# Optimization experiments

Hardware: AMD Instinct MI355X
Metric: run time of the kernel (lower is better)

Reference implementation:

```python
import jax, jax.numpy as jnp
import numpy as np

B, T, SZ, H = 16, 512, 512, 8
HD = SZ // H
D0, STD, GAMMA = 6.3, 1.4, 2.0
MAX_RPE = 16

def _dwconv(x, w):
    # depthwise conv1d, kernel 5, pad 2, groups=C, no bias; x: [B,T,C], w: [C,1,5]
    y = jax.lax.conv_general_dilated(x.transpose(0, 2, 1), w, (1,), [(2, 2)],
        dimension_numbers=('NCH', 'OIH', 'NCH'), feature_group_count=x.shape[-1])
    return y.transpose(0, 2, 1)

def _forward(mask, key, value, query, Wq, bq, Wk, bk, Wv, bv, Wcq, Wck, Wcv, Wgq, bgq, Wgk, bgk, Wgv, bgv, WmD, bmD, rpe_table, Wo, bo):
    q = query @ Wq.T + bq
    k = key @ Wk.T + bk
    v = value @ Wv.T + bv
    xn = key  # x_norm := key in the original forward
    # gated depthwise-conv context injection (qkv_context=[1,1,1], fuse='gate')
    qc = _dwconv(xn, Wcq)
    g = jax.nn.sigmoid(jnp.concatenate([q, qc], -1) @ Wgq.T + bgq)
    q = (1 - g) * q + g * qc
    kc = _dwconv(xn, Wck)
    g = jax.nn.sigmoid(jnp.concatenate([k, kc], -1) @ Wgk.T + bgk)
    k = (1 - g) * k + g * kc
    vc = _dwconv(xn, Wcv)
    g = jax.nn.sigmoid(jnp.concatenate([v, vc], -1) @ Wgv.T + bgv)
    v = (1 - g) * v + g * vc
    # learned Gaussian width: mod_D='head_share', mod_src='Q'
    off = (q @ WmD.T + bmD)[..., 0]                       # [B,T]
    m_D = D0 + 2.0 * STD * jnp.tanh(off / GAMMA)          # [B,T]
    qh = q.reshape(B, T, H, HD).transpose(0, 2, 1, 3) / jnp.sqrt(jnp.float32(HD))
    kh = k.reshape(B, T, H, HD).transpose(0, 2, 1, 3)
    vh = v.reshape(B, T, H, HD).transpose(0, 2, 1, 3)
    scores = jnp.einsum('bhqd,bhkd->bhqk', qh, kh)        # [B,H,T,T]
    idx = jnp.arange(T)
    d_int = idx[:, None] - idx[None, :]                   # i - j
    rd = jnp.clip(-d_int, -MAX_RPE, MAX_RPE) + MAX_RPE    # rpe indices [T,T]
    rpe = rpe_table[rd]                                   # [T,T,2*HD]
    rpe_k, rpe_v = rpe[..., :HD], rpe[..., HD:]
    scores = scores + jnp.einsum('bhqd,qkd->bhqk', qh, rpe_k)
    dist = d_int.astype(jnp.float32)
    scores = scores - dist ** 2 / (m_D[:, None, :, None] ** 2 / 2.0)
    scores = jnp.where(mask[:, None, :, :], -jnp.inf, scores)
    attn = jax.nn.softmax(scores, axis=-1)                # dropout is identity at eval
    ctx = jnp.einsum('bhqk,bhkd->bhqd', attn, vh) + jnp.einsum('bhqk,qkd->bhqd', attn, rpe_v)
    out = ctx.transpose(0, 2, 1, 3).reshape(B, T, SZ) @ Wo.T + bo
    return out

def setup_inputs():
    rng = jax.random.key(0)
    ks = jax.random.split(rng, 20)
    s = 0.02
    lin = lambda k, o, i: jax.random.normal(k, (o, i), jnp.float32) * s
    lengths = jax.random.randint(ks[3], (B,), T // 2, T + 1)
    mask = (jnp.arange(T)[None, :] >= lengths[:, None])[:, None, :]  # [B,1,T], True = pad
    return {
        'key': jax.random.normal(ks[0], (B, T, SZ), jnp.float32),
        'value': jax.random.normal(ks[1], (B, T, SZ), jnp.float32),
        'query': jax.random.normal(ks[2], (B, T, SZ), jnp.float32),
        'mask': mask,
        'Wq': lin(ks[4], SZ, SZ), 'bq': jnp.zeros((SZ,), jnp.float32),
        'Wk': lin(ks[5], SZ, SZ), 'bk': jnp.zeros((SZ,), jnp.float32),
        'Wv': lin(ks[6], SZ, SZ), 'bv': jnp.zeros((SZ,), jnp.float32),
        'Wcq': jax.random.normal(ks[7], (SZ, 1, 5), jnp.float32) * s,
        'Wck': jax.random.normal(ks[8], (SZ, 1, 5), jnp.float32) * s,
        'Wcv': jax.random.normal(ks[9], (SZ, 1, 5), jnp.float32) * s,
        'Wgq': lin(ks[10], 1, 2 * SZ), 'bgq': jnp.zeros((1,), jnp.float32),
        'Wgk': lin(ks[11], 1, 2 * SZ), 'bgk': jnp.zeros((1,), jnp.float32),
        'Wgv': lin(ks[12], 1, 2 * SZ), 'bgv': jnp.zeros((1,), jnp.float32),
        'WmD': lin(ks[13], 1, SZ), 'bmD': jnp.zeros((1,), jnp.float32),
        'rpe_table': jax.random.normal(ks[14], (2 * MAX_RPE + 1, 2 * HD), jnp.float32) * s,
        'Wo': lin(ks[15], SZ, SZ), 'bo': jnp.zeros((SZ,), jnp.float32),
    }

def reference(key, value, query, mask, Wq, bq, Wk, bk, Wv, bv, Wcq, Wck, Wcv, Wgq, bgq, Wgk, bgk, Wgv, bgv, WmD, bmD, rpe_table, Wo, bo):
    return _forward(mask, key, value, query, Wq, bq, Wk, bk, Wv, bv, Wcq, Wck, Wcv, Wgq, bgq, Wgk, bgk, Wgv, bgv, WmD, bmD, rpe_table, Wo, bo)
```

## Files before the change

kernel.cpp:

```cpp
#include <hip/hip_runtime.h>
#include <math.h>

#define NB 16
#define NT 512
#define NSZ 512
#define NH 8
#define NHD 64
#define MAXR 16

#define C_D0 6.3f
#define C_STD 1.4f
#define C_GAMMA 2.0f

#define NEGINF (-1e30f)
#define LOG2E 1.4426950408889634f
#define C1F   0.18033688011112042f

typedef unsigned short u16;
typedef __attribute__((ext_vector_type(8))) short bf16x8;
typedef __attribute__((ext_vector_type(4))) float f32x4;
typedef __attribute__((ext_vector_type(8))) unsigned short u16x8;

__device__ __forceinline__ u16 f2b(float f) {
    union { float f; unsigned int u; } c; c.f = f;
    unsigned int u = c.u + 0x7FFFu + ((c.u >> 16) & 1u);
    return (u16)(u >> 16);
}
__device__ __forceinline__ float b2f(u16 h) {
    union { unsigned int u; float f; } c; c.u = ((unsigned int)h) << 16;
    return c.f;
}

#if __has_builtin(__builtin_amdgcn_exp2f)
__device__ __forceinline__ float exp2_fast(float x) { return __builtin_amdgcn_exp2f(x); }
#else
__device__ __forceinline__ float exp2_fast(float x) { return exp2f(x); }
#endif

#define GL2LDS(gp, lp) __builtin_amdgcn_global_load_lds( \
    (const __attribute__((address_space(1))) void*)(gp), \
    (__attribute__((address_space(3))) void*)(lp), 16, 0, 0)

#define SWU(r, c) ((((r) * 8) + ((c) ^ ((r) & 7))) * 8)

__global__ __launch_bounds__(256) void cvt4_bf16(
    const float* __restrict__ s0, const float* __restrict__ s1,
    const float* __restrict__ s2, const float* __restrict__ s3,
    u16* __restrict__ d0, u16* __restrict__ d1,
    u16* __restrict__ d2, u16* __restrict__ d3, int n)
{
    const float* s; u16* d;
    switch (blockIdx.y) {
        case 0: s = s0; d = d0; break;
        case 1: s = s1; d = d1; break;
        case 2: s = s2; d = d2; break;
        default: s = s3; d = d3; break;
    }
    int i = (blockIdx.x * 256 + threadIdx.x) * 8;
    if (i >= n) return;
    float4 a = *(const float4*)&s[i];
    float4 b = *(const float4*)&s[i + 4];
    u16x8 v;
    v[0]=f2b(a.x); v[1]=f2b(a.y); v[2]=f2b(a.z); v[3]=f2b(a.w);
    v[4]=f2b(b.x); v[5]=f2b(b.y); v[6]=f2b(b.z); v[7]=f2b(b.w);
    *(u16x8*)&d[i] = v;
}

__global__ __launch_bounds__(256) void wprep(
    const float* __restrict__ Wcq, const float* __restrict__ Wck,
    const float* __restrict__ Wcv, float* __restrict__ WcT)
{
    const int z = blockIdx.y;
    const float* src = z == 0 ? Wcq : (z == 1 ? Wck : Wcv);
    int idx = blockIdx.x * 256 + threadIdx.x;
    if (idx >= 2560) return;
    int c = idx / 5, j = idx % 5;
    WcT[(size_t)z * 2560 + j * 512 + c] = src[idx];
}

__global__ __launch_bounds__(256) void gemm_qkv(
    const float* __restrict__ A0, const float* __restrict__ A1, const float* __restrict__ A2,
    const u16* __restrict__ Wc,
    const float* __restrict__ bq, const float* __restrict__ bk, const float* __restrict__ bv,
    u16* __restrict__ pkv)
{
    __shared__ u16 Al[128 * 32];
    __shared__ u16 Bl[128 * 32];
    const int z = blockIdx.z;
    const float* A = z == 0 ? A0 : (z == 1 ? A1 : A2);
    const u16* W = Wc + (size_t)z * NSZ * NSZ;
    const float* bias = z == 0 ? bq : (z == 1 ? bk : bv);
    const int tid = threadIdx.x;
    const int m0 = blockIdx.x * 128;
    const int n0 = blockIdx.y * 128;
    const int w = tid >> 6, lane = tid & 63;
    const int wm = (w >> 1) * 64, wn = (w & 1) * 64;
    const int fr = lane & 15, fk = lane >> 4;

    f32x4 acc[4][4] = {};
    for (int k0 = 0; k0 < NSZ; k0 += 32) {
        float4 a0[2], a1[2];
        #pragma unroll
        for (int p = 0; p < 2; ++p) {
            int s = tid + p * 256;
            int row = s >> 2, cb = s & 3;
            const float* ga = &A[(size_t)(m0 + row) * NSZ + k0 + cb * 8];
            a0[p] = *(const float4*)ga;
            a1[p] = *(const float4*)(ga + 4);
            GL2LDS(&W[(size_t)(n0 + row) * NSZ + k0 + cb * 8], &Bl[s * 8]);
        }
        #pragma unroll
        for (int p = 0; p < 2; ++p) {
            int s = tid + p * 256;
            u16x8 v;
            v[0]=f2b(a0[p].x); v[1]=f2b(a0[p].y); v[2]=f2b(a0[p].z); v[3]=f2b(a0[p].w);
            v[4]=f2b(a1[p].x); v[5]=f2b(a1[p].y); v[6]=f2b(a1[p].z); v[7]=f2b(a1[p].w);
            *(u16x8*)&Al[s * 8] = v;
        }
        __syncthreads();
        bf16x8 af[4], bfr[4];
        #pragma unroll
        for (int mf = 0; mf < 4; ++mf)
            af[mf] = *(const bf16x8*)&Al[(wm + mf * 16 + fr) * 32 + fk * 8];
        #pragma unroll
        for (int nf = 0; nf < 4; ++nf)
            bfr[nf] = *(const bf16x8*)&Bl[(wn + nf * 16 + fr) * 32 + fk * 8];
        #pragma unroll
        for (int mf = 0; mf < 4; ++mf)
            #pragma unroll
            for (int nf = 0; nf < 4; ++nf)
                acc[mf][nf] = __builtin_amdgcn_mfma_f32_16x16x32_bf16(
                    af[mf], bfr[nf], acc[mf][nf], 0, 0, 0);
        __syncthreads();
    }
    #pragma unroll
    for (int mf = 0; mf < 4; ++mf) {
        #pragma unroll
        for (int nf = 0; nf < 4; ++nf) {
            int col = n0 + wn + nf * 16 + fr;
            float bvv = bias[col];
            #pragma unroll
            for (int r = 0; r < 4; ++r) {
                int rowg = m0 + wm + mf * 16 + fk * 4 + r;
                pkv[(size_t)rowg * 1536 + z * 512 + col] = f2b(acc[mf][nf][r] + bvv);
            }
        }
    }
}

__global__ __launch_bounds__(256) void gemm_out(
    const u16* __restrict__ A, const u16* __restrict__ W,
    const float* __restrict__ bias, float* __restrict__ Cout, int M, int N, int K)
{
    __shared__ u16 Al[64 * 32];
    __shared__ u16 Bl[128 * 32];
    const int tid = threadIdx.x;
    const int m0 = blockIdx.x * 64;
    const int n0 = blockIdx.y * 128;
    const int w = tid >> 6, lane = tid & 63;
    const int wm = (w >> 1) * 32, wn = (w & 1) * 64;
    const int fr = lane & 15, fk = lane >> 4;

    f32x4 acc[2][4] = {};
    for (int k0 = 0; k0 < K; k0 += 32) {
        {
            int row = tid >> 2, cb = tid & 3;
            GL2LDS(&A[(size_t)(m0 + row) * K + k0 + cb * 8], &Al[tid * 8]);
        }
        #pragma unroll
        for (int p = 0; p < 2; ++p) {
            int s = tid + p * 256;
            int row = s >> 2, cb = s & 3;
            GL2LDS(&W[(size_t)(n0 + row) * K + k0 + cb * 8], &Bl[s * 8]);
        }
        __syncthreads();
        bf16x8 af[2], bfr[4];
        #pragma unroll
        for (int mf = 0; mf < 2; ++mf)
            af[mf] = *(const bf16x8*)&Al[(wm + mf * 16 + fr) * 32 + fk * 8];
        #pragma unroll
        for (int nf = 0; nf < 4; ++nf)
            bfr[nf] = *(const bf16x8*)&Bl[(wn + nf * 16 + fr) * 32 + fk * 8];
        #pragma unroll
        for (int mf = 0; mf < 2; ++mf)
            #pragma unroll
            for (int nf = 0; nf < 4; ++nf)
                acc[mf][nf] = __builtin_amdgcn_mfma_f32_16x16x32_bf16(
                    af[mf], bfr[nf], acc[mf][nf], 0, 0, 0);
        __syncthreads();
    }
    #pragma unroll
    for (int mf = 0; mf < 2; ++mf) {
        #pragma unroll
        for (int nf = 0; nf < 4; ++nf) {
            int col = n0 + wn + nf * 16 + fr;
            float bv = bias[col];
            #pragma unroll
            for (int r = 0; r < 4; ++r) {
                int rowg = m0 + wm + mf * 16 + fk * 4 + r;
                Cout[(size_t)rowg * N + col] = acc[mf][nf][r] + bv;
            }
        }
    }
}

__global__ void conv_gate_all(
    const float* __restrict__ xn, u16* __restrict__ pkv,
    const float* __restrict__ WcT,
    const float* __restrict__ Wgq, const float* __restrict__ bgq,
    const float* __restrict__ Wgk, const float* __restrict__ bgk,
    const float* __restrict__ Wgv, const float* __restrict__ bgv,
    const float* __restrict__ WmD, const float* __restrict__ bmD,
    float* __restrict__ mD)
{
    const int w = threadIdx.x >> 6, lane = threadIdx.x & 63;
    const int bt = blockIdx.x * 4 + w;
    const int b = bt >> 9, tpos = bt & (NT - 1);
    const int c0 = lane * 8;

    float x[5][8];
    #pragma unroll
    for (int j = 0; j < 5; ++j) {
        int tt = tpos + j - 2;
        if (tt >= 0 && tt < NT) {
            const float4* xp = (const float4*)&xn[((size_t)(b*NT + tt))*NSZ + c0];
            float4 u0 = xp[0], u1 = xp[1];
            x[j][0]=u0.x; x[j][1]=u0.y; x[j][2]=u0.z; x[j][3]=u0.w;
            x[j][4]=u1.x; x[j][5]=u1.y; x[j][6]=u1.z; x[j][7]=u1.w;
        } else {
            #pragma unroll
            for (int i = 0; i < 8; ++i) x[j][i] = 0.f;
        }
    }
    float aq[8] = {}, ak[8] = {}, av[8] = {};
    #pragma unroll
    for (int j = 0; j < 5; ++j) {
        const float* wq = &WcT[j * 512 + c0];
        const float* wk = &WcT[2560 + j * 512 + c0];
        const float* wv = &WcT[5120 + j * 512 + c0];
        float4 q0 = *(const float4*)wq, q1 = *(const float4*)(wq + 4);
        float4 k0 = *(const float4*)wk, k1 = *(const float4*)(wk + 4);
        float4 v0 = *(const float4*)wv, v1 = *(const float4*)(wv + 4);
        float wq8[8] = {q0.x,q0.y,q0.z,q0.w,q1.x,q1.y,q1.z,q1.w};
        float wk8[8] = {k0.x,k0.y,k0.z,k0.w,k1.x,k1.y,k1.z,k1.w};
        float wv8[8] = {v0.x,v0.y,v0.z,v0.w,v1.x,v1.y,v1.z,v1.w};
        #pragma unroll
        for (int i = 0; i < 8; ++i) {
            aq[i] += x[j][i] * wq8[i];
            ak[i] += x[j][i] * wk8[i];
            av[i] += x[j][i] * wv8[i];
        }
    }
    const size_t rb = (size_t)bt * 1536;
    u16x8 q8 = *(const u16x8*)&pkv[rb + c0];
    u16x8 k8 = *(const u16x8*)&pkv[rb + 512 + c0];
    u16x8 v8 = *(const u16x8*)&pkv[rb + 1024 + c0];

    float gql[8], gqh[8], gkl[8], gkh[8], gvl[8], gvh[8];
    {
        float4 a0 = *(const float4*)&Wgq[c0],      a1 = *(const float4*)&Wgq[c0 + 4];
        float4 a2 = *(const float4*)&Wgq[512 + c0], a3 = *(const float4*)&Wgq[512 + c0 + 4];
        gql[0]=a0.x;gql[1]=a0.y;gql[2]=a0.z;gql[3]=a0.w;gql[4]=a1.x;gql[5]=a1.y;gql[6]=a1.z;gql[7]=a1.w;
        gqh[0]=a2.x;gqh[1]=a2.y;gqh[2]=a2.z;gqh[3]=a2.w;gqh[4]=a3.x;gqh[5]=a3.y;gqh[6]=a3.z;gqh[7]=a3.w;
        float4 b0 = *(const float4*)&Wgk[c0],      b1 = *(const float4*)&Wgk[c0 + 4];
        float4 b2 = *(const float4*)&Wgk[512 + c0], b3 = *(const float4*)&Wgk[512 + c0 + 4];
        gkl[0]=b0.x;gkl[1]=b0.y;gkl[2]=b0.z;gkl[3]=b0.w;gkl[4]=b1.x;gkl[5]=b1.y;gkl[6]=b1.z;gkl[7]=b1.w;
        gkh[0]=b2.x;gkh[1]=b2.y;gkh[2]=b2.z;gkh[3]=b2.w;gkh[4]=b3.x;gkh[5]=b3.y;gkh[6]=b3.z;gkh[7]=b3.w;
        float4 c0v = *(const float4*)&Wgv[c0],      c1v = *(const float4*)&Wgv[c0 + 4];
        float4 c2v = *(const float4*)&Wgv[512 + c0], c3v = *(const float4*)&Wgv[512 + c0 + 4];
        gvl[0]=c0v.x;gvl[1]=c0v.y;gvl[2]=c0v.z;gvl[3]=c0v.w;gvl[4]=c1v.x;gvl[5]=c1v.y;gvl[6]=c1v.z;gvl[7]=c1v.w;
        gvh[0]=c2v.x;gvh[1]=c2v.y;gvh[2]=c2v.z;gvh[3]=c2v.w;gvh[4]=c3v.x;gvh[5]=c3v.y;gvh[6]=c3v.z;gvh[7]=c3v.w;
    }
    float sq = 0.f, sk = 0.f, sv = 0.f;
    #pragma unroll
    for (int i = 0; i < 8; ++i) {
        sq += b2f(q8[i]) * gql[i] + aq[i] * gqh[i];
        sk += b2f(k8[i]) * gkl[i] + ak[i] * gkh[i];
        sv += b2f(v8[i]) * gvl[i] + av[i] * gvh[i];
    }
    #pragma unroll
    for (int o = 1; o < 64; o <<= 1) {
        sq += __shfl_xor(sq, o, 64);
        sk += __shfl_xor(sk, o, 64);
        sv += __shfl_xor(sv, o, 64);
    }
    float gq = 1.f / (1.f + expf(-(sq + bgq[0])));
    float gk = 1.f / (1.f + expf(-(sk + bgk[0])));
    float gv = 1.f / (1.f + expf(-(sv + bgv[0])));

    float wm8[8];
    {
        float4 m0 = *(const float4*)&WmD[c0], m1 = *(const float4*)&WmD[c0 + 4];
        wm8[0]=m0.x;wm8[1]=m0.y;wm8[2]=m0.z;wm8[3]=m0.w;wm8[4]=m1.x;wm8[5]=m1.y;wm8[6]=m1.z;wm8[7]=m1.w;
    }
    u16x8 oq8, ok8, ov8;
    float smd = 0.f;
    #pragma unroll
    for (int i = 0; i < 8; ++i) {
        float oq = (1.f - gq) * b2f(q8[i]) + gq * aq[i];
        oq8[i] = f2b(oq);
        ok8[i] = f2b((1.f - gk) * b2f(k8[i]) + gk * ak[i]);
        ov8[i] = f2b((1.f - gv) * b2f(v8[i]) + gv * av[i]);
        smd += oq * wm8[i];
    }
    *(u16x8*)&pkv[rb + c0]        = oq8;
    *(u16x8*)&pkv[rb + 512 + c0]  = ok8;
    *(u16x8*)&pkv[rb + 1024 + c0] = ov8;
    #pragma unroll
    for (int o = 1; o < 64; o <<= 1) smd += __shfl_xor(smd, o, 64);
    if (lane == 0)
        mD[bt] = C_D0 + 2.f * C_STD * tanhf((smd + bmD[0]) / C_GAMMA);
}

__global__ __launch_bounds__(256) void vtrans(
    const u16* __restrict__ pkv, u16* __restrict__ vpT)
{
    __shared__ u16 lt[64][72];
    const int t0 = blockIdx.x * 64;
    const int h = blockIdx.y, b = blockIdx.z;
    const int tid = threadIdx.x;
    #pragma unroll
    for (int p = 0; p < 2; ++p) {
        int s = tid + p * 256;
        int t = s >> 3, c8 = s & 7;
        u16x8 v = *(const u16x8*)&pkv[((size_t)(b*NT + t0 + t))*1536 + 1024 + h*NHD + c8*8];
        *(u16x8*)&lt[t][c8 * 8] = v;
    }
    __syncthreads();
    #pragma unroll
    for (int p = 0; p < 2; ++p) {
        int s = tid + p * 256;
        int d = s >> 3, c8 = s & 7;
        u16x8 o;
        #pragma unroll
        for (int j = 0; j < 8; ++j) o[j] = lt[c8 * 8 + j][d];
        *(u16x8*)&vpT[((size_t)((b*NH + h)*NHD + d))*NT + t0 + c8*8] = o;
    }
}

__global__ __launch_bounds__(256) void attn_mfma(
    const u16* __restrict__ pkv, const u16* __restrict__ vpT,
    const float* __restrict__ mD, const int* __restrict__ mask,
    const float* __restrict__ rpe, u16* __restrict__ cxh)
{
    __shared__ __align__(16) char smem[38144];
    u16*  QP    = (u16*)(smem);
    u16*  Kl    = (u16*)(smem + 8192);
    u16*  Vl    = (u16*)(smem + 16384);
    u16*  rpk   = (u16*)(smem + 16384);
    u16*  rvl16 = (u16*)(smem + 8192);
    u16*  qdrl  = (u16*)(smem + 24576);
    float* wbufl= (float*)(smem + 29184);
    float* inv2s= (float*)(smem + 37888);

    const int tid  = threadIdx.x;
    const int lane = tid & 63;
    const int w    = tid >> 6;
    const int wq0  = w * 16;
    const int fr   = lane & 15;
    const int fq   = lane >> 4;
    const int b    = blockIdx.x >> 3;
    const int h    = blockIdx.x & 7;
    const int q0   = blockIdx.y * 64;

    const size_t qbase  = ((size_t)(b*NT + q0)) * 1536 + h * NHD;
    const size_t kbaseg = ((size_t)b * NT) * 1536 + 512 + h * NHD;
    const size_t vbaseg = ((size_t)((b*NH + h) * NHD)) * NT;

    int Lm = 512;
    #pragma unroll
    for (int j = 0; j < 8; ++j) {
        if (mask[b * NT + lane + 64 * j]) Lm = min(Lm, lane + 64 * j);
    }
    #pragma unroll
    for (int o = 1; o < 64; o <<= 1) Lm = min(Lm, __shfl_xor(Lm, o, 64));
    const int L = Lm;
    const int w0 = max(0, min(q0 - 32, L - 128));

    int r_[2], cs_[2];
    u16x8 qreg[2], kreg[2], vreg[2];
    #pragma unroll
    for (int p = 0; p < 2; ++p) {
        int s = tid + p * 256;
        r_[p] = s >> 3; cs_[p] = s & 7;
        qreg[p] = *(const u16x8*)(pkv + qbase  + (size_t)r_[p] * 1536 + cs_[p] * 8);
        kreg[p] = *(const u16x8*)(pkv + kbaseg + (size_t)(w0 + r_[p]) * 1536 + cs_[p] * 8);
        vreg[p] = *(const u16x8*)(vpT + vbaseg + (size_t)r_[p] * NT + w0 + cs_[p] * 8);
    }
    #pragma unroll
    for (int p = 0; p < 2; ++p) {
        *(u16x8*)(QP + SWU(r_[p], cs_[p])) = qreg[p];
        *(u16x8*)(Kl + SWU(r_[p], cs_[p])) = kreg[p];
    }
    for (int idx = tid; idx < 264; idx += 256) {
        int r = idx >> 3, c = idx & 7;
        float4 f0 = *(const float4*)&rpe[r * 128 + c * 8];
        float4 f1 = *(const float4*)&rpe[r * 128 + c * 8 + 4];
        u16x8 vv;
        vv[0]=f2b(f0.x); vv[1]=f2b(f0.y); vv[2]=f2b(f0.z); vv[3]=f2b(f0.w);
        vv[4]=f2b(f1.x); vv[5]=f2b(f1.y); vv[6]=f2b(f1.z); vv[7]=f2b(f1.w);
        *(u16x8*)(rpk + SWU(r, c)) = vv;
    }
    if (tid < 120) {
        u16x8 vv = {0,0,0,0,0,0,0,0};
        *(u16x8*)(rpk + (((33 + (tid >> 3)) * 8) + (tid & 7)) * 8) = vv;
    }
    if (tid < 64) {
        float md = mD[b * NT + q0 + tid];
        inv2s[tid] = 2.f * LOG2E / (md * md);
    }
    for (int i = tid; i < 64 * 34; i += 256) wbufl[i] = 0.f;
    __syncthreads();

    bf16x8 aq0 = *(const bf16x8*)(QP + SWU(wq0 + fr, fq));
    bf16x8 aq1 = *(const bf16x8*)(QP + SWU(wq0 + fr, 4 + fq));

    {
        f32x4 qd[3] = {};
        #pragma unroll
        for (int nf = 0; nf < 3; ++nf) {
            bf16x8 b0 = *(const bf16x8*)(rpk + SWU(nf * 16 + fr, fq));
            bf16x8 b1 = *(const bf16x8*)(rpk + SWU(nf * 16 + fr, 4 + fq));
            qd[nf] = __builtin_amdgcn_mfma_f32_16x16x32_bf16(aq0, b0, qd[nf], 0, 0, 0);
            qd[nf] = __builtin_amdgcn_mfma_f32_16x16x32_bf16(aq1, b1, qd[nf], 0, 0, 0);
        }
        #pragma unroll
        for (int nf = 0; nf < 3; ++nf) {
            int rd = nf * 16 + fr;
            if (rd < 33) {
                #pragma unroll
                for (int r = 0; r < 4; ++r)
                    qdrl[(wq0 + fq * 4 + r) * 36 + rd] = f2b(qd[nf][r]);
            }
        }
    }
    __syncthreads();
    #pragma unroll
    for (int p = 0; p < 2; ++p)
        *(u16x8*)(Vl + SWU(r_[p], cs_[p])) = vreg[p];

    f32x4 O[4] = {};
    float m2[4] = {NEGINF, NEGINF, NEGINF, NEGINF};
    float li[4] = {};

    #pragma unroll
    for (int t = 0; t < 2; ++t) {
        const int kb = w0 + t * 64;
        const bool pre = (t == 0);
        u16x8 kreg2[2], vreg2[2];
        if (pre) {
            const int kn = kb + 64;
            #pragma unroll
            for (int p = 0; p < 2; ++p) {
                kreg2[p] = *(const u16x8*)(pkv + kbaseg + (size_t)(kn + r_[p]) * 1536 + cs_[p] * 8);
                vreg2[p] = *(const u16x8*)(vpT + vbaseg + (size_t)r_[p] * NT + kn + cs_[p] * 8);
            }
        }
        int mk[4];
        #pragma unroll
        for (int nf = 0; nf < 4; ++nf) mk[nf] = (kb + nf * 16 + fr) >= L;

        f32x4 s_[4] = {};
        #pragma unroll
        for (int nf = 0; nf < 4; ++nf) {
            bf16x8 b0 = *(const bf16x8*)(Kl + SWU(nf * 16 + fr, fq));
            bf16x8 b1 = *(const bf16x8*)(Kl + SWU(nf * 16 + fr, 4 + fq));
            s_[nf] = __builtin_amdgcn_mfma_f32_16x16x32_bf16(aq0, b0, s_[nf], 0, 0, 0);
            s_[nf] = __builtin_amdgcn_mfma_f32_16x16x32_bf16(aq1, b1, s_[nf], 0, 0, 0);
        }
        const bool leftfar  = (kb + 79 <= q0);
        const bool rightfar = (kb >= q0 + 79);
        const bool mid = !leftfar && !rightfar;

        float p_[4][4], alpha[4], rsum_[4], ls_[4], rs_[4];
        #pragma unroll
        for (int r = 0; r < 4; ++r) {
            const int lq = wq0 + fq * 4 + r;
            const int qg = q0 + lq;
            const float iv = inv2s[lq];
            const float qf = leftfar ? b2f(qdrl[lq * 36]) : (rightfar ? b2f(qdrl[lq * 36 + 32]) : 0.f);
            float mx = NEGINF;
            #pragma unroll
            for (int nf = 0; nf < 4; ++nf) {
                const int kg = kb + nf * 16 + fr;
                float sc;
                if (mk[nf]) sc = NEGINF;
                else {
                    float qr = mid ? b2f(qdrl[lq * 36 + (min(max(kg - qg, -MAXR), MAXR) + MAXR)]) : qf;
                    float fd = (float)(qg - kg);
                    sc = (s_[nf][r] + qr) * C1F - fd * fd * iv;
                }
                p_[r][nf] = sc;
                mx = fmaxf(mx, sc);
            }
            mx = fmaxf(mx, __shfl_xor(mx, 1, 64));
            mx = fmaxf(mx, __shfl_xor(mx, 2, 64));
            mx = fmaxf(mx, __shfl_xor(mx, 4, 64));
            mx = fmaxf(mx, __shfl_xor(mx, 8, 64));
            float mn = fmaxf(m2[r], mx);
            alpha[r] = exp2_fast(m2[r] - mn);
            m2[r] = mn;
            float rsum = 0.f, ls = 0.f, rs = 0.f;
            #pragma unroll
            for (int nf = 0; nf < 4; ++nf) {
                float pv = exp2_fast(p_[r][nf] - mn);
                p_[r][nf] = pv;
                rsum += pv;
                if (mid) {
                    int kg = kb + nf * 16 + fr;
                    if (kg <= qg - MAXR) ls += pv;
                    else if (kg >= qg + MAXR) rs += pv;
                }
            }
            rsum += __shfl_xor(rsum, 1, 64); rsum += __shfl_xor(rsum, 2, 64);
            rsum += __shfl_xor(rsum, 4, 64); rsum += __shfl_xor(rsum, 8, 64);
            if (mid) {
                ls += __shfl_xor(ls, 1, 64); ls += __shfl_xor(ls, 2, 64);
                ls += __shfl_xor(ls, 4, 64); ls += __shfl_xor(ls, 8, 64);
                rs += __shfl_xor(rs, 1, 64); rs += __shfl_xor(rs, 2, 64);
                rs += __shfl_xor(rs, 4, 64); rs += __shfl_xor(rs, 8, 64);
            }
            li[r] = li[r] * alpha[r] + rsum;
            rsum_[r] = rsum; ls_[r] = ls; rs_[r] = rs;
        }
        #pragma unroll
        for (int nf = 0; nf < 4; ++nf) {
            O[nf][0] *= alpha[0]; O[nf][1] *= alpha[1];
            O[nf][2] *= alpha[2]; O[nf][3] *= alpha[3];
        }
        #pragma unroll
        for (int r = 0; r < 4; ++r) {
            int lq = wq0 + fq * 4 + r;
            if (alpha[r] != 1.f) {
                for (int c = fr; c < 33; c += 16) wbufl[lq * 34 + c] *= alpha[r];
            }
        }
        if (fr == 0) {
            #pragma unroll
            for (int r = 0; r < 4; ++r) {
                int lq = wq0 + fq * 4 + r;
                if (leftfar)       wbufl[lq * 34]      += rsum_[r];
                else if (rightfar) wbufl[lq * 34 + 32] += rsum_[r];
                else { wbufl[lq * 34] += ls_[r]; wbufl[lq * 34 + 32] += rs_[r]; }
            }
        }
        if (mid) {
            #pragma unroll
            for (int r = 0; r < 4; ++r) {
                int lq = wq0 + fq * 4 + r, qg = q0 + lq;
                #pragma unroll
                for (int nf = 0; nf < 4; ++nf) {
                    int d = kb + nf * 16 + fr - qg;
                    if (d > -MAXR && d < MAXR) wbufl[lq * 34 + d + MAXR] += p_[r][nf];
                }
            }
        }
        #pragma unroll
        for (int r = 0; r < 4; ++r) {
            int lq = wq0 + fq * 4 + r;
            #pragma unroll
            for (int nf = 0; nf < 4; ++nf) {
                int k = nf * 16 + fr;
                QP[lq * 64 + (((k >> 3) ^ (lq & 7)) << 3) + (k & 7)] = f2b(p_[r][nf]);
            }
        }
        __syncthreads();
        if (pre) {
            #pragma unroll
            for (int p = 0; p < 2; ++p)
                *(u16x8*)(Kl + SWU(r_[p], cs_[p])) = kreg2[p];
        }
        bf16x8 ap0 = *(const bf16x8*)(QP + SWU(wq0 + fr, fq));
        bf16x8 ap1 = *(const bf16x8*)(QP + SWU(wq0 + fr, 4 + fq));
        #pragma unroll
        for (int nf = 0; nf < 4; ++nf) {
            bf16x8 v0 = *(const bf16x8*)(Vl + SWU(nf * 16 + fr, fq));
            bf16x8 v1 = *(const bf16x8*)(Vl + SWU(nf * 16 + fr, 4 + fq));
            O[nf] = __builtin_amdgcn_mfma_f32_16x16x32_bf16(ap0, v0, O[nf], 0, 0, 0);
            O[nf] = __builtin_amdgcn_mfma_f32_16x16x32_bf16(ap1, v1, O[nf], 0, 0, 0);
        }
        __syncthreads();
        if (pre) {
            #pragma unroll
            for (int p = 0; p < 2; ++p)
                *(u16x8*)(Vl + SWU(r_[p], cs_[p])) = vreg2[p];
        }
    }

    for (int idx = tid; idx < 264; idx += 256) {
        int r = idx >> 3, c = idx & 7;
        float4 f0 = *(const float4*)&rpe[r * 128 + 64 + c * 8];
        float4 f1 = *(const float4*)&rpe[r * 128 + 64 + c * 8 + 4];
        u16x8 vv;
        vv[0]=f2b(f0.x); vv[1]=f2b(f0.y); vv[2]=f2b(f0.z); vv[3]=f2b(f0.w);
        vv[4]=f2b(f1.x); vv[5]=f2b(f1.y); vv[6]=f2b(f1.z); vv[7]=f2b(f1.w);
        *(u16x8*)(rvl16 + (r * 8 + c) * 8) = vv;
    }
    #pragma unroll
    for (int p = 0; p < 2; ++p) {
        int r = r_[p], cs = cs_[p];
        u16x8 vv;
        #pragma unroll
        for (int j = 0; j < 8; ++j) {
            int col = cs * 8 + j;
            vv[j] = (col < 34) ? f2b(wbufl[r * 34 + col]) : (u16)0;
        }
        *(u16x8*)(QP + SWU(r, cs)) = vv;
    }
    __syncthreads();
    #pragma unroll
    for (int p = 0; p < 2; ++p) {
        int d = r_[p], cs = cs_[p];
        u16x8 vv;
        #pragma unroll
        for (int j = 0; j < 8; ++j) {
            int rd = cs * 8 + j;
            vv[j] = (rd < 33) ? rvl16[rd * 64 + d] : (u16)0;
        }
        *(u16x8*)(Vl + SWU(d, cs)) = vv;
    }
    __syncthreads();
    {
        bf16x8 aw0 = *(const bf16x8*)(QP + SWU(wq0 + fr, fq));
        bf16x8 aw1 = *(const bf16x8*)(QP + SWU(wq0 + fr, 4 + fq));
        #pragma unroll
        for (int nf = 0; nf < 4; ++nf) {
            bf16x8 b0 = *(const bf16x8*)(Vl + SWU(nf * 16 + fr, fq));
            bf16x8 b1 = *(const bf16x8*)(Vl + SWU(nf * 16 + fr, 4 + fq));
            O[nf] = __builtin_amdgcn_mfma_f32_16x16x32_bf16(aw0, b0, O[nf], 0, 0, 0);
            O[nf] = __builtin_amdgcn_mfma_f32_16x16x32_bf16(aw1, b1, O[nf], 0, 0, 0);
        }
    }
    float invl[4];
    #pragma unroll
    for (int r = 0; r < 4; ++r) invl[r] = 1.f / li[r];
    #pragma unroll
    for (int r = 0; r < 4; ++r) {
        int lq = wq0 + fq * 4 + r;
        #pragma unroll
        for (int nf = 0; nf < 4; ++nf)
            Kl[lq * 64 + nf * 16 + fr] = f2b(O[nf][r] * invl[r]);
    }
    __syncthreads();
    #pragma unroll
    for (int j = 0; j < 2; ++j) {
        int s = w * 128 + j * 64 + lane;
        int rr = s >> 3, c8 = s & 7;
        u16x8 vv = *(const u16x8*)(Kl + rr * 64 + c8 * 8);
        *(u16x8*)&cxh[((size_t)(b*NT + q0 + rr)) * 512 + h * NHD + c8 * 8] = vv;
    }
}

extern "C" void kernel_launch(void* const* d_in, const int* in_sizes, int n_in,
                              void* d_out, int out_size, void* d_ws, size_t ws_size,
                              hipStream_t stream) {
    const float* key   = (const float*)d_in[0];
    const float* value = (const float*)d_in[1];
    const float* query = (const float*)d_in[2];
    const int*   mask  = (const int*)d_in[3];
    const float* Wq  = (const float*)d_in[4];
    const float* bq  = (const float*)d_in[5];
    const float* Wk  = (const float*)d_in[6];
    const float* bk  = (const float*)d_in[7];
    const float* Wv  = (const float*)d_in[8];
    const float* bv  = (const float*)d_in[9];
    const float* Wcq = (const float*)d_in[10];
    const float* Wck = (const float*)d_in[11];
    const float* Wcv = (const float*)d_in[12];
    const float* Wgq = (const float*)d_in[13];
    const float* bgq = (const float*)d_in[14];
    const float* Wgk = (const float*)d_in[15];
    const float* bgk = (const float*)d_in[16];
    const float* Wgv = (const float*)d_in[17];
    const float* bgv = (const float*)d_in[18];
    const float* WmD = (const float*)d_in[19];
    const float* bmD = (const float*)d_in[20];
    const float* rpe = (const float*)d_in[21];
    const float* Wo  = (const float*)d_in[22];
    const float* bo  = (const float*)d_in[23];
    float* out = (float*)d_out;

    const size_t NTOK = (size_t)NB * NT;
    const size_t NE   = NTOK * NSZ;
    const size_t NW   = (size_t)NSZ * NSZ;

    u16* ws16 = (u16*)d_ws;
    u16* pkv  = ws16;
    u16* wcat = pkv + NTOK * 1536;
    u16* woh  = wcat + 3 * NW;
    u16* vpT  = woh + NW;
    u16* cxh  = vpT + NE;
    float* mDb = (float*)(cxh + NE);
    float* WcT = mDb + NTOK;

    cvt4_bf16<<<dim3((unsigned)(NW/8/256), 4), 256, 0, stream>>>(
        Wq, Wk, Wv, Wo, wcat, wcat + NW, wcat + 2*NW, woh, (int)NW);
    wprep<<<dim3(10, 3), 256, 0, stream>>>(Wcq, Wck, Wcv, WcT);

    gemm_qkv<<<dim3(64, 4, 3), 256, 0, stream>>>(
        query, key, value, wcat, bq, bk, bv, pkv);

    conv_gate_all<<<(int)(NTOK / 4), 256, 0, stream>>>(
        key, pkv, WcT, Wgq, bgq, Wgk, bgk, Wgv, bgv, WmD, bmD, mDb);

    vtrans<<<dim3(8, 8, 16), 256, 0, stream>>>(pkv, vpT);

    attn_mfma<<<dim3(128, 8), 256, 0, stream>>>(pkv, vpT, mDb, mask, rpe, cxh);

    gemm_out<<<dim3(128, 4), 256, 0, stream>>>(cxh, woh, bo, out, (int)NTOK, NSZ, NSZ);
}
```

Baseline: 116.6 us.

## Single-pass 128-key window attention and smaller-M tiles for QKV GEMM

The attention kernel now loads the whole 128-key window of K and V into shared memory at once and does a single softmax pass. This replaces the two-tile online-softmax loop with its rescaling, register prefetch and extra barriers. Relative-position bucket weights go directly to a bf16 LDS buffer instead of a float accumulator, and the rpe_v table is read straight from global memory. The QKV GEMM tile shrinks from 128 to 64 rows, doubling the grid for better occupancy, at the cost of about 70KB of LDS per attention block, which may lower attention occupancy.

```diff
diff --git a/kernel.cpp b/kernel.cpp
--- a/kernel.cpp
+++ b/kernel.cpp
@@ -42,6 +42,7 @@
     (__attribute__((address_space(3))) void*)(lp), 16, 0, 0)
 
 #define SWU(r, c) ((((r) * 8) + ((c) ^ ((r) & 7))) * 8)
+#define SWU16(r, c) ((((r) * 16) + ((c) ^ ((r) & 7))) * 8)
 
 __global__ __launch_bounds__(256) void cvt4_bf16(
     const float* __restrict__ s0, const float* __restrict__ s1,
@@ -84,49 +85,50 @@
     const float* __restrict__ bq, const float* __restrict__ bk, const float* __restrict__ bv,
     u16* __restrict__ pkv)
 {
-    __shared__ u16 Al[128 * 32];
+    __shared__ u16 Al[64 * 32];
     __shared__ u16 Bl[128 * 32];
     const int z = blockIdx.z;
     const float* A = z == 0 ? A0 : (z == 1 ? A1 : A2);
     const u16* W = Wc + (size_t)z * NSZ * NSZ;
     const float* bias = z == 0 ? bq : (z == 1 ? bk : bv);
     const int tid = threadIdx.x;
-    const int m0 = blockIdx.x * 128;
+    const int m0 = blockIdx.x * 64;
     const int n0 = blockIdx.y * 128;
     const int w = tid >> 6, lane = tid & 63;
-    const int wm = (w >> 1) * 64, wn = (w & 1) * 64;
+    const int wm = (w >> 1) * 32, wn = (w & 1) * 64;
     const int fr = lane & 15, fk = lane >> 4;
 
-    f32x4 acc[4][4] = {};
+    f32x4 acc[2][4] = {};
     for (int k0 = 0; k0 < NSZ; k0 += 32) {
-        float4 a0[2], a1[2];
+        float4 a0, a1;
+        {
+            int row = tid >> 2, cb = tid & 3;
+            const float* ga = &A[(size_t)(m0 + row) * NSZ + k0 + cb * 8];
+            a0 = *(const float4*)ga;
+            a1 = *(const float4*)(ga + 4);
+        }
         #pragma unroll
         for (int p = 0; p < 2; ++p) {
             int s = tid + p * 256;
             int row = s >> 2, cb = s & 3;
-            const float* ga = &A[(size_t)(m0 + row) * NSZ + k0 + cb * 8];
-            a0[p] = *(const float4*)ga;
-            a1[p] = *(const float4*)(ga + 4);
             GL2LDS(&W[(size_t)(n0 + row) * NSZ + k0 + cb * 8], &Bl[s * 8]);
         }
-        #pragma unroll
-        for (int p = 0; p < 2; ++p) {
-            int s = tid + p * 256;
+        {
             u16x8 v;
-            v[0]=f2b(a0[p].x); v[1]=f2b(a0[p].y); v[2]=f2b(a0[p].z); v[3]=f2b(a0[p].w);
-            v[4]=f2b(a1[p].x); v[5]=f2b(a1[p].y); v[6]=f2b(a1[p].z); v[7]=f2b(a1[p].w);
-            *(u16x8*)&Al[s * 8] = v;
+            v[0]=f2b(a0.x); v[1]=f2b(a0.y); v[2]=f2b(a0.z); v[3]=f2b(a0.w);
+            v[4]=f2b(a1.x); v[5]=f2b(a1.y); v[6]=f2b(a1.z); v[7]=f2b(a1.w);
+            *(u16x8*)&Al[tid * 8] = v;
         }
         __syncthreads();
-        bf16x8 af[4], bfr[4];
-        #pragma unroll
-        for (int mf = 0; mf < 4; ++mf)
+        bf16x8 af[2], bfr[4];
+        #pragma unroll
+        for (int mf = 0; mf < 2; ++mf)
             af[mf] = *(const bf16x8*)&Al[(wm + mf * 16 + fr) * 32 + fk * 8];
         #pragma unroll
         for (int nf = 0; nf < 4; ++nf)
             bfr[nf] = *(const bf16x8*)&Bl[(wn + nf * 16 + fr) * 32 + fk * 8];
         #pragma unroll
-        for (int mf = 0; mf < 4; ++mf)
+        for (int mf = 0; mf < 2; ++mf)
             #pragma unroll
             for (int nf = 0; nf < 4; ++nf)
                 acc[mf][nf] = __builtin_amdgcn_mfma_f32_16x16x32_bf16(
@@ -134,7 +136,7 @@
         __syncthreads();
     }
     #pragma unroll
-    for (int mf = 0; mf < 4; ++mf) {
+    for (int mf = 0; mf < 2; ++mf) {
         #pragma unroll
         for (int nf = 0; nf < 4; ++nf) {
             int col = n0 + wn + nf * 16 + fr;
@@ -343,15 +345,15 @@
     const float* __restrict__ mD, const int* __restrict__ mask,
     const float* __restrict__ rpe, u16* __restrict__ cxh)
 {
-    __shared__ __align__(16) char smem[38144];
-    u16*  QP    = (u16*)(smem);
+    __shared__ __align__(16) char smem[70400];
+    u16*  Ql    = (u16*)(smem);
     u16*  Kl    = (u16*)(smem + 8192);
-    u16*  Vl    = (u16*)(smem + 16384);
-    u16*  rpk   = (u16*)(smem + 16384);
-    u16*  rvl16 = (u16*)(smem + 8192);
-    u16*  qdrl  = (u16*)(smem + 24576);
-    float* wbufl= (float*)(smem + 29184);
-    float* inv2s= (float*)(smem + 37888);
+    u16*  Vl    = (u16*)(smem + 24576);
+    u16*  Pl    = (u16*)(smem + 40960);
+    u16*  rpk   = (u16*)(smem + 40960);
+    u16*  wA16  = (u16*)(smem + 57344);
+    u16*  qdrl  = (u16*)(smem + 65536);
+    float* inv2s= (float*)(smem + 70144);
 
     const int tid  = threadIdx.x;
     const int lane = tid & 63;
@@ -377,20 +379,26 @@
     const int L = Lm;
     const int w0 = max(0, min(q0 - 32, L - 128));
 
-    int r_[2], cs_[2];
-    u16x8 qreg[2], kreg[2], vreg[2];
     #pragma unroll
     for (int p = 0; p < 2; ++p) {
         int s = tid + p * 256;
-        r_[p] = s >> 3; cs_[p] = s & 7;
-        qreg[p] = *(const u16x8*)(pkv + qbase  + (size_t)r_[p] * 1536 + cs_[p] * 8);
-        kreg[p] = *(const u16x8*)(pkv + kbaseg + (size_t)(w0 + r_[p]) * 1536 + cs_[p] * 8);
-        vreg[p] = *(const u16x8*)(vpT + vbaseg + (size_t)r_[p] * NT + w0 + cs_[p] * 8);
-    }
-    #pragma unroll
-    for (int p = 0; p < 2; ++p) {
-        *(u16x8*)(QP + SWU(r_[p], cs_[p])) = qreg[p];
-        *(u16x8*)(Kl + SWU(r_[p], cs_[p])) = kreg[p];
+        int r = s >> 3, c = s & 7;
+        u16x8 v = *(const u16x8*)(pkv + qbase + (size_t)r * 1536 + c * 8);
+        *(u16x8*)(Ql + SWU(r, c)) = v;
+    }
+    #pragma unroll
+    for (int p = 0; p < 4; ++p) {
+        int s = tid + p * 256;
+        int r = s >> 3, c = s & 7;
+        u16x8 v = *(const u16x8*)(pkv + kbaseg + (size_t)(w0 + r) * 1536 + c * 8);
+        *(u16x8*)(Kl + SWU(r, c)) = v;
+    }
+    #pragma unroll
+    for (int p = 0; p < 4; ++p) {
+        int s = tid + p * 256;
+        int d = s >> 4, cc = s & 15;
+        u16x8 v = *(const u16x8*)(vpT + vbaseg + (size_t)d * NT + w0 + cc * 8);
+        *(u16x8*)(Vl + SWU16(d, cc)) = v;
     }
     for (int idx = tid; idx < 264; idx += 256) {
         int r = idx >> 3, c = idx & 7;
@@ -405,15 +413,19 @@
         u16x8 vv = {0,0,0,0,0,0,0,0};
         *(u16x8*)(rpk + (((33 + (tid >> 3)) * 8) + (tid & 7)) * 8) = vv;
     }
+    {
+        u16x8 z = {0,0,0,0,0,0,0,0};
+        #pragma unroll
+        for (int p = 0; p < 2; ++p) *(u16x8*)(wA16 + (tid + p * 256) * 8) = z;
+    }
     if (tid < 64) {
         float md = mD[b * NT + q0 + tid];
         inv2s[tid] = 2.f * LOG2E / (md * md);
     }
-    for (int i = tid; i < 64 * 34; i += 256) wbufl[i] = 0.f;
     __syncthreads();
 
-    bf16x8 aq0 = *(const bf16x8*)(QP + SWU(wq0 + fr, fq));
-    bf16x8 aq1 = *(const bf16x8*)(QP + SWU(wq0 + fr, 4 + fq));
+    bf16x8 aq0 = *(const bf16x8*)(Ql + SWU(wq0 + fr, fq));
+    bf16x8 aq1 = *(const bf16x8*)(Ql + SWU(wq0 + fr, 4 + fq));
 
     {
         f32x4 qd[3] = {};
@@ -435,194 +447,110 @@
         }
     }
     __syncthreads();
-    #pragma unroll
-    for (int p = 0; p < 2; ++p)
-        *(u16x8*)(Vl + SWU(r_[p], cs_[p])) = vreg[p];
+
+    f32x4 s_[8] = {};
+    #pragma unroll
+    for (int nf = 0; nf < 8; ++nf) {
+        bf16x8 b0 = *(const bf16x8*)(Kl + SWU(nf * 16 + fr, fq));
+        bf16x8 b1 = *(const bf16x8*)(Kl + SWU(nf * 16 + fr, 4 + fq));
+        s_[nf] = __builtin_amdgcn_mfma_f32_16x16x32_bf16(aq0, b0, s_[nf], 0, 0, 0);
+        s_[nf] = __builtin_amdgcn_mfma_f32_16x16x32_bf16(aq1, b1, s_[nf], 0, 0, 0);
+    }
+
+    float li[4];
+    #pragma unroll
+    for (int r = 0; r < 4; ++r) {
+        const int lq = wq0 + fq * 4 + r;
+        const int qg = q0 + lq;
+        const float iv = inv2s[lq];
+        float sc[8];
+        float mx = NEGINF;
+        #pragma unroll
+        for (int nf = 0; nf < 8; ++nf) {
+            const int kg = w0 + nf * 16 + fr;
+            float v;
+            if (kg >= L) v = NEGINF;
+            else {
+                int rd = min(max(kg - qg, -MAXR), MAXR) + MAXR;
+                float qr = b2f(qdrl[lq * 36 + rd]);
+                float fd = (float)(qg - kg);
+                v = (s_[nf][r] + qr) * C1F - fd * fd * iv;
+            }
+            sc[nf] = v;
+            mx = fmaxf(mx, v);
+        }
+        mx = fmaxf(mx, __shfl_xor(mx, 1, 64));
+        mx = fmaxf(mx, __shfl_xor(mx, 2, 64));
+        mx = fmaxf(mx, __shfl_xor(mx, 4, 64));
+        mx = fmaxf(mx, __shfl_xor(mx, 8, 64));
+        float rsum = 0.f, ls = 0.f, rs = 0.f;
+        #pragma unroll
+        for (int nf = 0; nf < 8; ++nf) {
+            const int kg = w0 + nf * 16 + fr;
+            float pv = exp2_fast(sc[nf] - mx);
+            s_[nf][r] = pv;
+            rsum += pv;
+            int d = kg - qg;
+            if (d <= -MAXR) ls += pv;
+            else if (d >= MAXR) rs += pv;
+            else {
+                int bkt = d + MAXR;
+                wA16[(lq * 8 + ((bkt >> 3) ^ (lq & 7))) * 8 + (bkt & 7)] = f2b(pv);
+            }
+        }
+        rsum += __shfl_xor(rsum, 1, 64); rsum += __shfl_xor(rsum, 2, 64);
+        rsum += __shfl_xor(rsum, 4, 64); rsum += __shfl_xor(rsum, 8, 64);
+        ls += __shfl_xor(ls, 1, 64); ls += __shfl_xor(ls, 2, 64);
+        ls += __shfl_xor(ls, 4, 64); ls += __shfl_xor(ls, 8, 64);
+        rs += __shfl_xor(rs, 1, 64); rs += __shfl_xor(rs, 2, 64);
+        rs += __shfl_xor(rs, 4, 64); rs += __shfl_xor(rs, 8, 64);
+        li[r] = rsum;
+        if (fr == 0) {
+            wA16[(lq * 8 + (0 ^ (lq & 7))) * 8 + 0] = f2b(ls);
+            wA16[(lq * 8 + (4 ^ (lq & 7))) * 8 + 0] = f2b(rs);
+        }
+    }
+
+    #pragma unroll
+    for (int r = 0; r < 4; ++r) {
+        int lq = wq0 + fq * 4 + r;
+        #pragma unroll
+        for (int nf = 0; nf < 8; ++nf) {
+            int k = nf * 16 + fr;
+            int cc = k >> 3;
+            Pl[(lq * 16 + (cc ^ (lq & 7))) * 8 + (k & 7)] = f2b(s_[nf][r]);
+        }
+    }
 
     f32x4 O[4] = {};
-    float m2[4] = {NEGINF, NEGINF, NEGINF, NEGINF};
-    float li[4] = {};
-
-    #pragma unroll
-    for (int t = 0; t < 2; ++t) {
-        const int kb = w0 + t * 64;
-        const bool pre = (t == 0);
-        u16x8 kreg2[2], vreg2[2];
-        if (pre) {
-            const int kn = kb + 64;
-            #pragma unroll
-            for (int p = 0; p < 2; ++p) {
-                kreg2[p] = *(const u16x8*)(pkv + kbaseg + (size_t)(kn + r_[p]) * 1536 + cs_[p] * 8);
-                vreg2[p] = *(const u16x8*)(vpT + vbaseg + (size_t)r_[p] * NT + kn + cs_[p] * 8);
-            }
-        }
-        int mk[4];
-        #pragma unroll
-        for (int nf = 0; nf < 4; ++nf) mk[nf] = (kb + nf * 16 + fr) >= L;
-
-        f32x4 s_[4] = {};
+    #pragma unroll
+    for (int ks = 0; ks < 4; ++ks) {
+        bf16x8 ap = *(const bf16x8*)(Pl + ((wq0 + fr) * 16 + ((ks * 4 + fq) ^ (fr & 7))) * 8);
         #pragma unroll
         for (int nf = 0; nf < 4; ++nf) {
-            bf16x8 b0 = *(const bf16x8*)(Kl + SWU(nf * 16 + fr, fq));
-            bf16x8 b1 = *(const bf16x8*)(Kl + SWU(nf * 16 + fr, 4 + fq));
-            s_[nf] = __builtin_amdgcn_mfma_f32_16x16x32_bf16(aq0, b0, s_[nf], 0, 0, 0);
-            s_[nf] = __builtin_amdgcn_mfma_f32_16x16x32_bf16(aq1, b1, s_[nf], 0, 0, 0);
-        }
-        const bool leftfar  = (kb + 79 <= q0);
-        const bool rightfar = (kb >= q0 + 79);
-        const bool mid = !leftfar && !rightfar;
-
-        float p_[4][4], alpha[4], rsum_[4], ls_[4], rs_[4];
-        #pragma unroll
-        for (int r = 0; r < 4; ++r) {
-            const int lq = wq0 + fq * 4 + r;
-            const int qg = q0 + lq;
-            const float iv = inv2s[lq];
-            const float qf = leftfar ? b2f(qdrl[lq * 36]) : (rightfar ? b2f(qdrl[lq * 36 + 32]) : 0.f);
-            float mx = NEGINF;
-            #pragma unroll
-            for (int nf = 0; nf < 4; ++nf) {
-                const int kg = kb + nf * 16 + fr;
-                float sc;
-                if (mk[nf]) sc = NEGINF;
-                else {
-                    float qr = mid ? b2f(qdrl[lq * 36 + (min(max(kg - qg, -MAXR), MAXR) + MAXR)]) : qf;
-                    float fd = (float)(qg - kg);
-                    sc = (s_[nf][r] + qr) * C1F - fd * fd * iv;
-                }
-                p_[r][nf] = sc;
-                mx = fmaxf(mx, sc);
-            }
-            mx = fmaxf(mx, __shfl_xor(mx, 1, 64));
-            mx = fmaxf(mx, __shfl_xor(mx, 2, 64));
-            mx = fmaxf(mx, __shfl_xor(mx, 4, 64));
-            mx = fmaxf(mx, __shfl_xor(mx, 8, 64));
-            float mn = fmaxf(m2[r], mx);
-            alpha[r] = exp2_fast(m2[r] - mn);
-            m2[r] = mn;
-            float rsum = 0.f, ls = 0.f, rs = 0.f;
-            #pragma unroll
-            for (int nf = 0; nf < 4; ++nf) {
-                float pv = exp2_fast(p_[r][nf] - mn);
-                p_[r][nf] = pv;
-                rsum += pv;
-                if (mid) {
-                    int kg = kb + nf * 16 + fr;
-                    if (kg <= qg - MAXR) ls += pv;
-                    else if (kg >= qg + MAXR) rs += pv;
-                }
-            }
-            rsum += __shfl_xor(rsum, 1, 64); rsum += __shfl_xor(rsum, 2, 64);
-            rsum += __shfl_xor(rsum, 4, 64); rsum += __shfl_xor(rsum, 8, 64);
-            if (mid) {
-                ls += __shfl_xor(ls, 1, 64); ls += __shfl_xor(ls, 2, 64);
-                ls += __shfl_xor(ls, 4, 64); ls += __shfl_xor(ls, 8, 64);
-                rs += __shfl_xor(rs, 1, 64); rs += __shfl_xor(rs, 2, 64);
-                rs += __shfl_xor(rs, 4, 64); rs += __shfl_xor(rs, 8, 64);
-            }
-            li[r] = li[r] * alpha[r] + rsum;
-            rsum_[r] = rsum; ls_[r] = ls; rs_[r] = rs;
-        }
-        #pragma unroll
-        for (int nf = 0; nf < 4; ++nf) {
-            O[nf][0] *= alpha[0]; O[nf][1] *= alpha[1];
-            O[nf][2] *= alpha[2]; O[nf][3] *= alpha[3];
-        }
-        #pragma unroll
-        for (int r = 0; r < 4; ++r) {
-            int lq = wq0 + fq * 4 + r;
-            if (alpha[r] != 1.f) {
-                for (int c = fr; c < 33; c += 16) wbufl[lq * 34 + c] *= alpha[r];
-            }
-        }
-        if (fr == 0) {
-            #pragma unroll
-            for (int r = 0; r < 4; ++r) {
-                int lq = wq0 + fq * 4 + r;
-                if (leftfar)       wbufl[lq * 34]      += rsum_[r];
-                else if (rightfar) wbufl[lq * 34 + 32] += rsum_[r];
-                else { wbufl[lq * 34] += ls_[r]; wbufl[lq * 34 + 32] += rs_[r]; }
-            }
-        }
-        if (mid) {
-            #pragma unroll
-            for (int r = 0; r < 4; ++r) {
-                int lq = wq0 + fq * 4 + r, qg = q0 + lq;
-                #pragma unroll
-                for (int nf = 0; nf < 4; ++nf) {
-                    int d = kb + nf * 16 + fr - qg;
-                    if (d > -MAXR && d < MAXR) wbufl[lq * 34 + d + MAXR] += p_[r][nf];
-                }
-            }
-        }
-        #pragma unroll
-        for (int r = 0; r < 4; ++r) {
-            int lq = wq0 + fq * 4 + r;
-            #pragma unroll
-            for (int nf = 0; nf < 4; ++nf) {
-                int k = nf * 16 + fr;
-                QP[lq * 64 + (((k >> 3) ^ (lq & 7)) << 3) + (k & 7)] = f2b(p_[r][nf]);
-            }
-        }
-        __syncthreads();
-        if (pre) {
-            #pragma unroll
-            for (int p = 0; p < 2; ++p)
-                *(u16x8*)(Kl + SWU(r_[p], cs_[p])) = kreg2[p];
-        }
-        bf16x8 ap0 = *(const bf16x8*)(QP + SWU(wq0 + fr, fq));
-        bf16x8 ap1 = *(const bf16x8*)(QP + SWU(wq0 + fr, 4 + fq));
-        #pragma unroll
-        for (int nf = 0; nf < 4; ++nf) {
-            bf16x8 v0 = *(const bf16x8*)(Vl + SWU(nf * 16 + fr, fq));
-            bf16x8 v1 = *(const bf16x8*)(Vl + SWU(nf * 16 + fr, 4 + fq));
-            O[nf] = __builtin_amdgcn_mfma_f32_16x16x32_bf16(ap0, v0, O[nf], 0, 0, 0);
-            O[nf] = __builtin_amdgcn_mfma_f32_16x16x32_bf16(ap1, v1, O[nf], 0, 0, 0);
-        }
-        __syncthreads();
-        if (pre) {
-            #pragma unroll
-            for (int p = 0; p < 2; ++p)
-                *(u16x8*)(Vl + SWU(r_[p], cs_[p])) = vreg2[p];
-        }
-    }
-
-    for (int idx = tid; idx < 264; idx += 256) {
-        int r = idx >> 3, c = idx & 7;
-        float4 f0 = *(const float4*)&rpe[r * 128 + 64 + c * 8];
-        float4 f1 = *(const float4*)&rpe[r * 128 + 64 + c * 8 + 4];
-        u16x8 vv;
-        vv[0]=f2b(f0.x); vv[1]=f2b(f0.y); vv[2]=f2b(f0.z); vv[3]=f2b(f0.w);
-        vv[4]=f2b(f1.x); vv[5]=f2b(f1.y); vv[6]=f2b(f1.z); vv[7]=f2b(f1.w);
-        *(u16x8*)(rvl16 + (r * 8 + c) * 8) = vv;
-    }
+            bf16x8 vf = *(const bf16x8*)(Vl + ((nf * 16 + fr) * 16 + ((ks * 4 + fq) ^ (fr & 7))) * 8);
+            O[nf] = __builtin_amdgcn_mfma_f32_16x16x32_bf16(ap, vf, O[nf], 0, 0, 0);
+        }
+    }
+    __syncthreads();
+
     #pragma unroll
     for (int p = 0; p < 2; ++p) {
-        int r = r_[p], cs = cs_[p];
-        u16x8 vv;
-        #pragma unroll
-        for (int j = 0; j < 8; ++j) {
-            int col = cs * 8 + j;
-            vv[j] = (col < 34) ? f2b(wbufl[r * 34 + col]) : (u16)0;
-        }
-        *(u16x8*)(QP + SWU(r, cs)) = vv;
-    }
-    __syncthreads();
-    #pragma unroll
-    for (int p = 0; p < 2; ++p) {
-        int d = r_[p], cs = cs_[p];
+        int s = tid + p * 256;
+        int d = s >> 3, cs = s & 7;
         u16x8 vv;
         #pragma unroll
         for (int j = 0; j < 8; ++j) {
             int rd = cs * 8 + j;
-            vv[j] = (rd < 33) ? rvl16[rd * 64 + d] : (u16)0;
+            vv[j] = (rd < 33) ? f2b(rpe[rd * 128 + 64 + d]) : (u16)0;
         }
         *(u16x8*)(Vl + SWU(d, cs)) = vv;
     }
     __syncthreads();
+
     {
-        bf16x8 aw0 = *(const bf16x8*)(QP + SWU(wq0 + fr, fq));
-        bf16x8 aw1 = *(const bf16x8*)(QP + SWU(wq0 + fr, 4 + fq));
+        bf16x8 aw0 = *(const bf16x8*)(wA16 + SWU(wq0 + fr, fq));
+        bf16x8 aw1 = *(const bf16x8*)(wA16 + SWU(wq0 + fr, 4 + fq));
         #pragma unroll
         for (int nf = 0; nf < 4; ++nf) {
             bf16x8 b0 = *(const bf16x8*)(Vl + SWU(nf * 16 + fr, fq));
@@ -639,14 +567,14 @@
         int lq = wq0 + fq * 4 + r;
         #pragma unroll
         for (int nf = 0; nf < 4; ++nf)
-            Kl[lq * 64 + nf * 16 + fr] = f2b(O[nf][r] * invl[r]);
+            Pl[lq * 64 + nf * 16 + fr] = f2b(O[nf][r] * invl[r]);
     }
     __syncthreads();
     #pragma unroll
     for (int j = 0; j < 2; ++j) {
         int s = w * 128 + j * 64 + lane;
         int rr = s >> 3, c8 = s & 7;
-        u16x8 vv = *(const u16x8*)(Kl + rr * 64 + c8 * 8);
+        u16x8 vv = *(const u16x8*)(Pl + rr * 64 + c8 * 8);
         *(u16x8*)&cxh[((size_t)(b*NT + q0 + rr)) * 512 + h * NHD + c8 * 8] = vv;
     }
 }
@@ -697,7 +625,7 @@
         Wq, Wk, Wv, Wo, wcat, wcat + NW, wcat + 2*NW, woh, (int)NW);
     wprep<<<dim3(10, 3), 256, 0, stream>>>(Wcq, Wck, Wcv, WcT);
 
-    gemm_qkv<<<dim3(64, 4, 3), 256, 0, stream>>>(
+    gemm_qkv<<<dim3(128, 4, 3), 256, 0, stream>>>(
         query, key, value, wcat, bq, bk, bv, pkv);
 
     conv_gate_all<<<(int)(NTOK / 4), 256, 0, stream>>>(
```

Result: no change. 115.6 us (-0.8%).
